# Performance work log

Hardware: AMD Instinct MI355X
Metric: run time of the kernel (lower is better)

Reference implementation:

```python
import jax, jax.numpy as jnp
import numpy as np

B, T, D, H = 2, 2048, 1024, 16
STD = 0.02

def setup_inputs() -> dict:
    key = jax.random.key(0)
    ks = jax.random.split(key, 5)
    x = jax.random.normal(ks[0], (B, T, D), dtype=jnp.float32)
    Wq = jax.random.normal(ks[1], (D, D), dtype=jnp.float32) * STD
    Wk = jax.random.normal(ks[2], (D, D), dtype=jnp.float32) * STD
    Wv = jax.random.normal(ks[3], (D, D), dtype=jnp.float32) * STD
    Wo = jax.random.normal(ks[4], (D, D), dtype=jnp.float32) * STD
    z = jnp.zeros((D,), dtype=jnp.float32)
    return {"x": x, "Wq": Wq, "bq": z, "Wk": Wk, "bk": z, "Wv": Wv, "bv": z, "Wo": Wo, "bo": z}

def _split(t, h):
    b, s, dm = t.shape
    return t.reshape(b, s, h, dm // h).transpose(0, 2, 1, 3)  # (B,h,T,d)

def reference(x, Wq, bq, Wk, bk, Wv, bv, Wo, bo):
    h = H
    # linear projections (nn.Linear: y = x @ W^T + b)
    q = _split(x @ Wq.T + bq, h)
    k = _split(x @ Wk.T + bk, h)
    v = _split(x @ Wv.T + bv, h)
    d_k = k.shape[-1]
    # scaled dot-product similarities (B,h,T,T)
    sim = jnp.einsum("bhqd,bhkd->bhqk", q, k) / jnp.sqrt(jnp.float32(d_k))
    # causal mask: upper triangle (excluding diag) filled with -inf
    Tq = sim.shape[-1]
    causal = jnp.tril(jnp.ones((Tq, Tq), dtype=bool))
    sim = jnp.where(causal, sim, -jnp.inf)
    attn = jax.nn.softmax(sim, axis=-1)
    ctx = jnp.einsum("bhqk,bhkd->bhqd", attn, v)  # (B,h,T,d)
    ctx = ctx.transpose(0, 2, 1, 3).reshape(x.shape[0], x.shape[1], -1)  # (B,T,D)
    return ctx @ Wo.T + bo
```

## Files before the change

### kernel.cpp

```cpp
#include <hip/hip_runtime.h>
#include <hip/hip_bf16.h>


typedef __attribute__((ext_vector_type(8))) short bf16x8;
typedef __attribute__((ext_vector_type(4))) float f32x4;

#define QSCALE 0.18033688011f

__device__ __forceinline__ int sniff_f32(const void* p) {
    const unsigned short* u = (const unsigned short*)p;
    int c = 0;
    for (int i = 0; i < 256; ++i) {
        int e = (u[i] >> 7) & 0xFF;
        c += (e >= 0x90) ? 1 : 0;
    }
    return c > 8;
}

__device__ __forceinline__ void async_copy16(const void* g, void* l) {
    __builtin_amdgcn_global_load_lds(
        (const __attribute__((address_space(1))) void*)g,
        (__attribute__((address_space(3))) void*)l, 16, 0, 0);
}

struct Cvt { const void* src; __hip_bfloat16* dst; int n; };
struct CvtPack { Cvt a[9]; };

__global__ __launch_bounds__(256) void cvt_bf16(CvtPack pk) {
    const Cvt c = pk.a[blockIdx.y];
    const int f32 = sniff_f32(c.src);
    const int stride = gridDim.x * 256 * 8;
    for (int idx = (blockIdx.x * 256 + threadIdx.x) * 8; idx < c.n; idx += stride) {
        if (f32) {
            const float* s = (const float*)c.src + idx;
            f32x4 a0 = *(const f32x4*)s;
            f32x4 a1 = *(const f32x4*)(s + 4);
            union { __hip_bfloat16 h[8]; bf16x8 v; } u;
#pragma unroll
            for (int e = 0; e < 4; e++) u.h[e]     = (__hip_bfloat16)a0[e];
#pragma unroll
            for (int e = 0; e < 4; e++) u.h[4 + e] = (__hip_bfloat16)a1[e];
            *(bf16x8*)&c.dst[idx] = u.v;
        } else {
            *(bf16x8*)&c.dst[idx] = *(const bf16x8*)((const __hip_bfloat16*)c.src + idx);
        }
    }
}

template <bool OF32>
__device__ __forceinline__ void gemm_async_body(
    const __hip_bfloat16* __restrict__ A, const __hip_bfloat16* __restrict__ W,
    const __hip_bfloat16* __restrict__ bias, void* __restrict__ C,
    int M, int N, int K, int bm, int bn, float outscale,
    __hip_bfloat16* sA, __hip_bfloat16* sB)
{
    const int tid  = threadIdx.x;
    const int wave = tid >> 6;
    const int lane = tid & 63;
    const int quad = lane >> 4;
    const int l15  = lane & 15;
    const int wr   = wave >> 1;
    const int wc   = wave & 1;

    const int srow = wave * 16 + (lane >> 2);
    const int scol = (lane & 3) * 8;
    const __hip_bfloat16* gA0 = A + (size_t)(bm + srow) * K + scol;
    const __hip_bfloat16* gB0 = W + (size_t)(bn + srow) * K + scol;
    __hip_bfloat16* sA0 = sA + wave * 512;
    __hip_bfloat16* sB0 = sB + wave * 512;

    f32x4 acc[4][4];
#pragma unroll
    for (int i = 0; i < 4; i++)
#pragma unroll
        for (int j = 0; j < 4; j++) acc[i][j] = (f32x4)0.0f;

    for (int k0 = 0; k0 < K; k0 += 32) {
        __syncthreads();
#pragma unroll
        for (int r = 0; r < 2; r++) {
            async_copy16(gA0 + (size_t)r * 64 * K + k0, sA0 + r * 2048);
            async_copy16(gB0 + (size_t)r * 64 * K + k0, sB0 + r * 2048);
        }
        __syncthreads();

        bf16x8 af[4], bf[4];
#pragma unroll
        for (int i = 0; i < 4; i++)
            af[i] = *(const bf16x8*)&sA[(wr * 64 + i * 16 + l15) * 32 + quad * 8];
#pragma unroll
        for (int j = 0; j < 4; j++)
            bf[j] = *(const bf16x8*)&sB[(wc * 64 + j * 16 + l15) * 32 + quad * 8];
#pragma unroll
        for (int i = 0; i < 4; i++)
#pragma unroll
            for (int j = 0; j < 4; j++)
                acc[i][j] = __builtin_amdgcn_mfma_f32_16x16x32_bf16(af[i], bf[j], acc[i][j], 0, 0, 0);
    }

    float bv[4];
#pragma unroll
    for (int j = 0; j < 4; j++)
        bv[j] = (float)bias[bn + wc * 64 + j * 16 + l15];
#pragma unroll
    for (int i = 0; i < 4; i++) {
#pragma unroll
        for (int j = 0; j < 4; j++) {
            int col = bn + wc * 64 + j * 16 + l15;
#pragma unroll
            for (int r = 0; r < 4; r++) {
                int row = bm + wr * 64 + i * 16 + quad * 4 + r;
                float v = (acc[i][j][r] + bv[j]) * outscale;
                if (OF32) ((float*)C)[(size_t)row * N + col] = v;
                else      ((__hip_bfloat16*)C)[(size_t)row * N + col] = (__hip_bfloat16)v;
            }
        }
    }
}

__global__ __launch_bounds__(256, 2) void qkv_gemm(
    const __hip_bfloat16* __restrict__ x,
    const __hip_bfloat16* __restrict__ Wq, const __hip_bfloat16* __restrict__ bq, __hip_bfloat16* __restrict__ Q,
    const __hip_bfloat16* __restrict__ Wk, const __hip_bfloat16* __restrict__ bk, __hip_bfloat16* __restrict__ Kb,
    const __hip_bfloat16* __restrict__ Wv, const __hip_bfloat16* __restrict__ bv, __hip_bfloat16* __restrict__ V,
    int M, int N, int K)
{
    __shared__ __hip_bfloat16 sA[128 * 32];
    __shared__ __hip_bfloat16 sB[128 * 32];
    const __hip_bfloat16* Wp; const __hip_bfloat16* bp; __hip_bfloat16* Cp; float sc;
    if (blockIdx.z == 0)      { Wp = Wq; bp = bq; Cp = Q;  sc = QSCALE; }
    else if (blockIdx.z == 1) { Wp = Wk; bp = bk; Cp = Kb; sc = 1.0f; }
    else                      { Wp = Wv; bp = bv; Cp = V;  sc = 1.0f; }
    gemm_async_body<false>(x, Wp, bp, Cp, M, N, K,
                           blockIdx.x * 128, blockIdx.y * 128, sc, sA, sB);
}

__global__ __launch_bounds__(256, 2) void out_gemm(
    const __hip_bfloat16* __restrict__ A, const __hip_bfloat16* __restrict__ W,
    const __hip_bfloat16* __restrict__ bias, const void* __restrict__ origW,
    void* __restrict__ C, int M, int N, int K)
{
    __shared__ __hip_bfloat16 sA[128 * 32];
    __shared__ __hip_bfloat16 sB[128 * 32];
    __shared__ int f32flag;
    if (threadIdx.x == 0) f32flag = sniff_f32(origW);
    __syncthreads();
    if (f32flag)
        gemm_async_body<true>(A, W, bias, C, M, N, K,
                              blockIdx.x * 128, blockIdx.y * 128, 1.0f, sA, sB);
    else
        gemm_async_body<false>(A, W, bias, C, M, N, K,
                               blockIdx.x * 128, blockIdx.y * 128, 1.0f, sA, sB);
}

__global__ __launch_bounds__(256, 2) void transpose_v(
    const __hip_bfloat16* __restrict__ V, __hip_bfloat16* __restrict__ VT,
    int T, int D, int H)
{
    __shared__ __hip_bfloat16 sT[64 * 72];
    const int tid = threadIdx.x;
    const int t0  = blockIdx.x * 64;
    const int h   = blockIdx.y;
    const int b   = blockIdx.z;

    for (int i = tid; i < 512; i += 256) {
        int t = i >> 3, d8 = (i & 7) * 8;
        *(bf16x8*)&sT[t * 72 + d8] =
            *(const bf16x8*)&V[((size_t)b * T + t0 + t) * D + h * 64 + d8];
    }
    __syncthreads();
    for (int i = tid; i < 512; i += 256) {
        int d = i >> 3, t8 = (i & 7) * 8;
        union { __hip_bfloat16 h[8]; bf16x8 v; } u;
#pragma unroll
        for (int e = 0; e < 8; e++) u.h[e] = sT[(t8 + e) * 72 + d];
        *(bf16x8*)&VT[(((size_t)b * H + h) * 64 + d) * T + t0 + t8] = u.v;
    }
}

#define PAD 68

__device__ __forceinline__ void tile_step(
    const __hip_bfloat16* __restrict__ sQx, __hip_bfloat16* __restrict__ sPw,
    const bf16x8 kfrag[2][4], const bf16x8 vfrag[2][4],
    f32x4 acc[4], float lacc[4],
    int diag, int wave, int quad, int l15)
{
    f32x4 s[4];
#pragma unroll
    for (int j = 0; j < 4; j++) s[j] = (f32x4)0.0f;
#pragma unroll
    for (int kk = 0; kk < 2; kk++) {
        bf16x8 a = *(const bf16x8*)&sQx[(wave * 16 + l15) * PAD + kk * 32 + quad * 8];
#pragma unroll
        for (int j = 0; j < 4; j++)
            s[j] = __builtin_amdgcn_mfma_f32_16x16x32_bf16(a, kfrag[kk][j], s[j], 0, 0, 0);
    }
    if (diag) {
        const int qrow = wave * 16 + quad * 4;
#pragma unroll
        for (int j = 0; j < 4; j++) {
            int key = j * 16 + l15;
#pragma unroll
            for (int r = 0; r < 4; r++)
                if (key > qrow + r) s[j][r] = -1e30f;
        }
    }
#pragma unroll
    for (int j = 0; j < 4; j++) {
#pragma unroll
        for (int r = 0; r < 4; r++) {
            float p = exp2f(s[j][r]);
            lacc[r] += p;
            sPw[(quad * 4 + r) * PAD + j * 16 + l15] = (__hip_bfloat16)p;
        }
    }
#pragma unroll
    for (int kk = 0; kk < 2; kk++) {
        bf16x8 a = *(const bf16x8*)&sPw[l15 * PAD + kk * 32 + quad * 8];
#pragma unroll
        for (int j = 0; j < 4; j++)
            acc[j] = __builtin_amdgcn_mfma_f32_16x16x32_bf16(a, vfrag[kk][j], acc[j], 0, 0, 0);
    }
}

__global__ __launch_bounds__(256, 2) void attn_causal(
    const __hip_bfloat16* __restrict__ Q,
    const __hip_bfloat16* __restrict__ K,
    const __hip_bfloat16* __restrict__ VT,
    __hip_bfloat16* __restrict__ O,
    int T, int D, int H)
{
    __shared__ __hip_bfloat16 sQ[2][64 * PAD];
    __shared__ __hip_bfloat16 sK[64 * PAD];
    __shared__ __hip_bfloat16 sVT[64 * PAD];
    __shared__ __hip_bfloat16 sP[4][16 * PAD];

    const int tid  = threadIdx.x;
    const int wave = tid >> 6;
    const int lane = tid & 63;
    const int quad = lane >> 4;
    const int l15  = lane & 15;

    const int NT  = T >> 6;
    const int p   = blockIdx.x;
    const int qtA = p;
    const int qtB = NT - 1 - p;
    const int h   = blockIdx.y;
    const int b   = blockIdx.z;
    const size_t headoff = (size_t)b * T * D + (size_t)h * 64;
    const size_t vtoff   = ((size_t)b * H + h) * 64 * (size_t)T;

    for (int i = tid; i < 1024; i += 256) {
        int tile = i >> 9, ii = i & 511;
        int row = ii >> 3, c8 = ii & 7;
        int qt = tile ? qtB : qtA;
        *(bf16x8*)&sQ[tile][row * PAD + c8 * 8] =
            *(const bf16x8*)&Q[headoff + (size_t)(qt * 64 + row) * D + c8 * 8];
    }

    f32x4 accA[4], accB[4];
#pragma unroll
    for (int j = 0; j < 4; j++) { accA[j] = (f32x4)0.0f; accB[j] = (f32x4)0.0f; }
    float lA[4] = {0.f, 0.f, 0.f, 0.f}, lB[4] = {0.f, 0.f, 0.f, 0.f};

    const int srow = tid >> 3;
    const int sc8  = (tid & 7) * 8;

    bf16x8 pk[2], pv[2];
#pragma unroll
    for (int u = 0; u < 2; u++) {
        int row = srow + u * 32;
        pk[u] = *(const bf16x8*)&K[headoff + (size_t)row * D + sc8];
        pv[u] = *(const bf16x8*)&VT[vtoff + (size_t)row * T + sc8];
    }

    for (int kt = 0; kt <= qtB; ++kt) {
        __syncthreads();
#pragma unroll
        for (int u = 0; u < 2; u++) {
            int row = srow + u * 32;
            *(bf16x8*)&sK[row * PAD + sc8]  = pk[u];
            *(bf16x8*)&sVT[row * PAD + sc8] = pv[u];
        }
        if (kt < qtB) {
#pragma unroll
            for (int u = 0; u < 2; u++) {
                int row = srow + u * 32;
                pk[u] = *(const bf16x8*)&K[headoff + (size_t)((kt + 1) * 64 + row) * D + sc8];
                pv[u] = *(const bf16x8*)&VT[vtoff + (size_t)row * T + (kt + 1) * 64 + sc8];
            }
        }
        __syncthreads();

        bf16x8 kfrag[2][4], vfrag[2][4];
#pragma unroll
        for (int kk = 0; kk < 2; kk++)
#pragma unroll
            for (int j = 0; j < 4; j++) {
                kfrag[kk][j] = *(const bf16x8*)&sK[(j * 16 + l15) * PAD + kk * 32 + quad * 8];
                vfrag[kk][j] = *(const bf16x8*)&sVT[(j * 16 + l15) * PAD + kk * 32 + quad * 8];
            }

        tile_step(sQ[1], sP[wave], kfrag, vfrag, accB, lB, kt == qtB, wave, quad, l15);
        if (kt <= qtA)
            tile_step(sQ[0], sP[wave], kfrag, vfrag, accA, lA, kt == qtA, wave, quad, l15);
    }

#pragma unroll
    for (int o = 1; o < 16; o <<= 1)
#pragma unroll
        for (int r = 0; r < 4; r++) {
            lA[r] += __shfl_xor(lA[r], o, 64);
            lB[r] += __shfl_xor(lB[r], o, 64);
        }

#pragma unroll
    for (int r = 0; r < 4; r++) {
        float iA = 1.0f / lA[r], iB = 1.0f / lB[r];
        int rowA = qtA * 64 + wave * 16 + quad * 4 + r;
        int rowB = qtB * 64 + wave * 16 + quad * 4 + r;
#pragma unroll
        for (int j = 0; j < 4; j++) {
            int col = j * 16 + l15;
            O[headoff + (size_t)rowA * D + col] = (__hip_bfloat16)(accA[j][r] * iA);
            O[headoff + (size_t)rowB * D + col] = (__hip_bfloat16)(accB[j][r] * iB);
        }
    }
}

extern "C" void kernel_launch(void* const* d_in, const int* in_sizes, int n_in,
                              void* d_out, int out_size, void* d_ws, size_t ws_size,
                              hipStream_t stream) {
    const int Bb = 2, T = 2048, D = 1024, H = 16;
    const int M = Bb * T;

    __hip_bfloat16* w = (__hip_bfloat16*)d_ws;
    __hip_bfloat16* Q   = w;
    __hip_bfloat16* Kb  = Q   + (size_t)M * D;
    __hip_bfloat16* Vb  = Kb  + (size_t)M * D;
    __hip_bfloat16* ctx = Vb  + (size_t)M * D;
    __hip_bfloat16* VT  = ctx + (size_t)M * D;
    __hip_bfloat16* xb  = VT  + (size_t)M * D;
    __hip_bfloat16* Wqb = xb  + (size_t)M * D;
    __hip_bfloat16* Wkb = Wqb + (size_t)D * D;
    __hip_bfloat16* Wvb = Wkb + (size_t)D * D;
    __hip_bfloat16* Wob = Wvb + (size_t)D * D;
    __hip_bfloat16* bqb = Wob + (size_t)D * D;
    __hip_bfloat16* bkb = bqb + D;
    __hip_bfloat16* bvb = bkb + D;
    __hip_bfloat16* bob = bvb + D;

    CvtPack pk;
    pk.a[0] = { d_in[0], xb,  M * D };
    pk.a[1] = { d_in[1], Wqb, D * D };
    pk.a[2] = { d_in[2], bqb, D };
    pk.a[3] = { d_in[3], Wkb, D * D };
    pk.a[4] = { d_in[4], bkb, D };
    pk.a[5] = { d_in[5], Wvb, D * D };
    pk.a[6] = { d_in[6], bvb, D };
    pk.a[7] = { d_in[7], Wob, D * D };
    pk.a[8] = { d_in[8], bob, D };

    cvt_bf16<<<dim3(512, 9), 256, 0, stream>>>(pk);
    qkv_gemm<<<dim3(M / 128, D / 128, 3), 256, 0, stream>>>(
        xb, Wqb, bqb, Q, Wkb, bkb, Kb, Wvb, bvb, Vb, M, D, D);
    transpose_v<<<dim3(T / 64, H, Bb), 256, 0, stream>>>(Vb, VT, T, D, H);
    attn_causal<<<dim3(T / 128, H, Bb), 256, 0, stream>>>(Q, Kb, VT, ctx, T, D, H);
    out_gemm<<<dim3(M / 128, D / 128), 256, 0, stream>>>(
        ctx, Wob, bob, d_in[7], d_out, M, D, D);
}
```

Baseline: 246.4 us.

## Split attention to one query tile per block and use 64-row output GEMM tiles

The causal attention kernel now handles a single 64-row query tile per block instead of a balanced pair (p, NT-1-p). That doubles the grid and raises the launch-bounds occupancy target to 4. Heads are split in two halves that walk the query tiles in opposite orders, so heavy and light blocks mix. K/V fragments are now read per MFMA rather than held in registers. The output GEMM gets a new 64x128-tile body, which doubles its block count for better CU fill, at the cost of more redundant K/V and weight loads and an uneven per-block workload in attention.

```diff
diff --git a/kernel.cpp b/kernel.cpp
--- a/kernel.cpp
+++ b/kernel.cpp
@@ -135,22 +135,88 @@
                            blockIdx.x * 128, blockIdx.y * 128, sc, sA, sB);
 }
 
+template <bool OF32>
+__device__ __forceinline__ void gemm64_body(
+    const __hip_bfloat16* __restrict__ A, const __hip_bfloat16* __restrict__ W,
+    const __hip_bfloat16* __restrict__ bias, void* __restrict__ C,
+    int M, int N, int K, int bm, int bn,
+    __hip_bfloat16* sA, __hip_bfloat16* sB)
+{
+    const int tid  = threadIdx.x;
+    const int wave = tid >> 6;
+    const int lane = tid & 63;
+    const int quad = lane >> 4;
+    const int l15  = lane & 15;
+
+    const int srow = wave * 16 + (lane >> 2);
+    const int scol = (lane & 3) * 8;
+    const __hip_bfloat16* gA0 = A + (size_t)(bm + srow) * K + scol;
+    const __hip_bfloat16* gB0 = W + (size_t)(bn + srow) * K + scol;
+    __hip_bfloat16* sA0 = sA + wave * 512;
+    __hip_bfloat16* sB0 = sB + wave * 512;
+
+    f32x4 acc[4][2];
+#pragma unroll
+    for (int i = 0; i < 4; i++)
+#pragma unroll
+        for (int j = 0; j < 2; j++) acc[i][j] = (f32x4)0.0f;
+
+    for (int k0 = 0; k0 < K; k0 += 32) {
+        __syncthreads();
+        async_copy16(gA0 + k0, sA0);
+#pragma unroll
+        for (int r = 0; r < 2; r++)
+            async_copy16(gB0 + (size_t)r * 64 * K + k0, sB0 + r * 2048);
+        __syncthreads();
+
+        bf16x8 af[4], bf[2];
+#pragma unroll
+        for (int i = 0; i < 4; i++)
+            af[i] = *(const bf16x8*)&sA[(i * 16 + l15) * 32 + quad * 8];
+#pragma unroll
+        for (int j = 0; j < 2; j++)
+            bf[j] = *(const bf16x8*)&sB[(wave * 32 + j * 16 + l15) * 32 + quad * 8];
+#pragma unroll
+        for (int i = 0; i < 4; i++)
+#pragma unroll
+            for (int j = 0; j < 2; j++)
+                acc[i][j] = __builtin_amdgcn_mfma_f32_16x16x32_bf16(af[i], bf[j], acc[i][j], 0, 0, 0);
+    }
+
+    float bv[2];
+#pragma unroll
+    for (int j = 0; j < 2; j++)
+        bv[j] = (float)bias[bn + wave * 32 + j * 16 + l15];
+#pragma unroll
+    for (int i = 0; i < 4; i++) {
+#pragma unroll
+        for (int j = 0; j < 2; j++) {
+            int col = bn + wave * 32 + j * 16 + l15;
+#pragma unroll
+            for (int r = 0; r < 4; r++) {
+                int row = bm + i * 16 + quad * 4 + r;
+                float v = acc[i][j][r] + bv[j];
+                if (OF32) ((float*)C)[(size_t)row * N + col] = v;
+                else      ((__hip_bfloat16*)C)[(size_t)row * N + col] = (__hip_bfloat16)v;
+            }
+        }
+    }
+}
+
 __global__ __launch_bounds__(256, 2) void out_gemm(
     const __hip_bfloat16* __restrict__ A, const __hip_bfloat16* __restrict__ W,
     const __hip_bfloat16* __restrict__ bias, const void* __restrict__ origW,
     void* __restrict__ C, int M, int N, int K)
 {
-    __shared__ __hip_bfloat16 sA[128 * 32];
+    __shared__ __hip_bfloat16 sA[64 * 32];
     __shared__ __hip_bfloat16 sB[128 * 32];
     __shared__ int f32flag;
     if (threadIdx.x == 0) f32flag = sniff_f32(origW);
     __syncthreads();
     if (f32flag)
-        gemm_async_body<true>(A, W, bias, C, M, N, K,
-                              blockIdx.x * 128, blockIdx.y * 128, 1.0f, sA, sB);
+        gemm64_body<true>(A, W, bias, C, M, N, K, blockIdx.x * 64, blockIdx.y * 128, sA, sB);
     else
-        gemm_async_body<false>(A, W, bias, C, M, N, K,
-                               blockIdx.x * 128, blockIdx.y * 128, 1.0f, sA, sB);
+        gemm64_body<false>(A, W, bias, C, M, N, K, blockIdx.x * 64, blockIdx.y * 128, sA, sB);
 }
 
 __global__ __launch_bounds__(256, 2) void transpose_v(
@@ -180,58 +246,14 @@
 
 #define PAD 68
 
-__device__ __forceinline__ void tile_step(
-    const __hip_bfloat16* __restrict__ sQx, __hip_bfloat16* __restrict__ sPw,
-    const bf16x8 kfrag[2][4], const bf16x8 vfrag[2][4],
-    f32x4 acc[4], float lacc[4],
-    int diag, int wave, int quad, int l15)
-{
-    f32x4 s[4];
-#pragma unroll
-    for (int j = 0; j < 4; j++) s[j] = (f32x4)0.0f;
-#pragma unroll
-    for (int kk = 0; kk < 2; kk++) {
-        bf16x8 a = *(const bf16x8*)&sQx[(wave * 16 + l15) * PAD + kk * 32 + quad * 8];
-#pragma unroll
-        for (int j = 0; j < 4; j++)
-            s[j] = __builtin_amdgcn_mfma_f32_16x16x32_bf16(a, kfrag[kk][j], s[j], 0, 0, 0);
-    }
-    if (diag) {
-        const int qrow = wave * 16 + quad * 4;
-#pragma unroll
-        for (int j = 0; j < 4; j++) {
-            int key = j * 16 + l15;
-#pragma unroll
-            for (int r = 0; r < 4; r++)
-                if (key > qrow + r) s[j][r] = -1e30f;
-        }
-    }
-#pragma unroll
-    for (int j = 0; j < 4; j++) {
-#pragma unroll
-        for (int r = 0; r < 4; r++) {
-            float p = exp2f(s[j][r]);
-            lacc[r] += p;
-            sPw[(quad * 4 + r) * PAD + j * 16 + l15] = (__hip_bfloat16)p;
-        }
-    }
-#pragma unroll
-    for (int kk = 0; kk < 2; kk++) {
-        bf16x8 a = *(const bf16x8*)&sPw[l15 * PAD + kk * 32 + quad * 8];
-#pragma unroll
-        for (int j = 0; j < 4; j++)
-            acc[j] = __builtin_amdgcn_mfma_f32_16x16x32_bf16(a, vfrag[kk][j], acc[j], 0, 0, 0);
-    }
-}
-
-__global__ __launch_bounds__(256, 2) void attn_causal(
+__global__ __launch_bounds__(256, 4) void attn_causal(
     const __hip_bfloat16* __restrict__ Q,
     const __hip_bfloat16* __restrict__ K,
     const __hip_bfloat16* __restrict__ VT,
     __hip_bfloat16* __restrict__ O,
     int T, int D, int H)
 {
-    __shared__ __hip_bfloat16 sQ[2][64 * PAD];
+    __shared__ __hip_bfloat16 sQ[64 * PAD];
     __shared__ __hip_bfloat16 sK[64 * PAD];
     __shared__ __hip_bfloat16 sVT[64 * PAD];
     __shared__ __hip_bfloat16 sP[4][16 * PAD];
@@ -242,27 +264,23 @@
     const int quad = lane >> 4;
     const int l15  = lane & 15;
 
-    const int NT  = T >> 6;
-    const int p   = blockIdx.x;
-    const int qtA = p;
-    const int qtB = NT - 1 - p;
-    const int h   = blockIdx.y;
-    const int b   = blockIdx.z;
+    const int NT = T >> 6;
+    const int qt = ((blockIdx.y >> 3) & 1) ? (NT - 1 - (int)blockIdx.x) : (int)blockIdx.x;
+    const int h  = blockIdx.y;
+    const int b  = blockIdx.z;
     const size_t headoff = (size_t)b * T * D + (size_t)h * 64;
     const size_t vtoff   = ((size_t)b * H + h) * 64 * (size_t)T;
 
-    for (int i = tid; i < 1024; i += 256) {
-        int tile = i >> 9, ii = i & 511;
-        int row = ii >> 3, c8 = ii & 7;
-        int qt = tile ? qtB : qtA;
-        *(bf16x8*)&sQ[tile][row * PAD + c8 * 8] =
+    for (int i = tid; i < 512; i += 256) {
+        int row = i >> 3, c8 = i & 7;
+        *(bf16x8*)&sQ[row * PAD + c8 * 8] =
             *(const bf16x8*)&Q[headoff + (size_t)(qt * 64 + row) * D + c8 * 8];
     }
 
-    f32x4 accA[4], accB[4];
-#pragma unroll
-    for (int j = 0; j < 4; j++) { accA[j] = (f32x4)0.0f; accB[j] = (f32x4)0.0f; }
-    float lA[4] = {0.f, 0.f, 0.f, 0.f}, lB[4] = {0.f, 0.f, 0.f, 0.f};
+    f32x4 acc_o[4];
+#pragma unroll
+    for (int j = 0; j < 4; j++) acc_o[j] = (f32x4)0.0f;
+    float lacc[4] = {0.f, 0.f, 0.f, 0.f};
 
     const int srow = tid >> 3;
     const int sc8  = (tid & 7) * 8;
@@ -275,7 +293,7 @@
         pv[u] = *(const bf16x8*)&VT[vtoff + (size_t)row * T + sc8];
     }
 
-    for (int kt = 0; kt <= qtB; ++kt) {
+    for (int kt = 0; kt <= qt; ++kt) {
         __syncthreads();
 #pragma unroll
         for (int u = 0; u < 2; u++) {
@@ -283,7 +301,7 @@
             *(bf16x8*)&sK[row * PAD + sc8]  = pk[u];
             *(bf16x8*)&sVT[row * PAD + sc8] = pv[u];
         }
-        if (kt < qtB) {
+        if (kt < qt) {
 #pragma unroll
             for (int u = 0; u < 2; u++) {
                 int row = srow + u * 32;
@@ -293,38 +311,64 @@
         }
         __syncthreads();
 
-        bf16x8 kfrag[2][4], vfrag[2][4];
-#pragma unroll
-        for (int kk = 0; kk < 2; kk++)
+        f32x4 s[4];
+#pragma unroll
+        for (int j = 0; j < 4; j++) s[j] = (f32x4)0.0f;
+#pragma unroll
+        for (int kk = 0; kk < 2; kk++) {
+            bf16x8 a = *(const bf16x8*)&sQ[(wave * 16 + l15) * PAD + kk * 32 + quad * 8];
 #pragma unroll
             for (int j = 0; j < 4; j++) {
-                kfrag[kk][j] = *(const bf16x8*)&sK[(j * 16 + l15) * PAD + kk * 32 + quad * 8];
-                vfrag[kk][j] = *(const bf16x8*)&sVT[(j * 16 + l15) * PAD + kk * 32 + quad * 8];
-            }
-
-        tile_step(sQ[1], sP[wave], kfrag, vfrag, accB, lB, kt == qtB, wave, quad, l15);
-        if (kt <= qtA)
-            tile_step(sQ[0], sP[wave], kfrag, vfrag, accA, lA, kt == qtA, wave, quad, l15);
+                bf16x8 bk8 = *(const bf16x8*)&sK[(j * 16 + l15) * PAD + kk * 32 + quad * 8];
+                s[j] = __builtin_amdgcn_mfma_f32_16x16x32_bf16(a, bk8, s[j], 0, 0, 0);
+            }
+        }
+
+        if (kt == qt) {
+            const int qrow = wave * 16 + quad * 4;
+#pragma unroll
+            for (int j = 0; j < 4; j++) {
+                int key = j * 16 + l15;
+#pragma unroll
+                for (int r = 0; r < 4; r++)
+                    if (key > qrow + r) s[j][r] = -1e30f;
+            }
+        }
+
+#pragma unroll
+        for (int j = 0; j < 4; j++) {
+#pragma unroll
+            for (int r = 0; r < 4; r++) {
+                float p = exp2f(s[j][r]);
+                lacc[r] += p;
+                sP[wave][(quad * 4 + r) * PAD + j * 16 + l15] = (__hip_bfloat16)p;
+            }
+        }
+#pragma unroll
+        for (int kk = 0; kk < 2; kk++) {
+            bf16x8 a = *(const bf16x8*)&sP[wave][l15 * PAD + kk * 32 + quad * 8];
+#pragma unroll
+            for (int j = 0; j < 4; j++) {
+                bf16x8 bv8 = *(const bf16x8*)&sVT[(j * 16 + l15) * PAD + kk * 32 + quad * 8];
+                acc_o[j] = __builtin_amdgcn_mfma_f32_16x16x32_bf16(a, bv8, acc_o[j], 0, 0, 0);
+            }
+        }
     }
 
 #pragma unroll
     for (int o = 1; o < 16; o <<= 1)
 #pragma unroll
-        for (int r = 0; r < 4; r++) {
-            lA[r] += __shfl_xor(lA[r], o, 64);
-            lB[r] += __shfl_xor(lB[r], o, 64);
-        }
+        for (int r = 0; r < 4; r++)
+            lacc[r] += __shfl_xor(lacc[r], o, 64);
 
 #pragma unroll
     for (int r = 0; r < 4; r++) {
-        float iA = 1.0f / lA[r], iB = 1.0f / lB[r];
-        int rowA = qtA * 64 + wave * 16 + quad * 4 + r;
-        int rowB = qtB * 64 + wave * 16 + quad * 4 + r;
+        float inv = 1.0f / lacc[r];
+        int row = qt * 64 + wave * 16 + quad * 4 + r;
 #pragma unroll
         for (int j = 0; j < 4; j++) {
             int col = j * 16 + l15;
-            O[headoff + (size_t)rowA * D + col] = (__hip_bfloat16)(accA[j][r] * iA);
-            O[headoff + (size_t)rowB * D + col] = (__hip_bfloat16)(accB[j][r] * iB);
+            O[headoff + (size_t)row * D + col] = (__hip_bfloat16)(acc_o[j][r] * inv);
         }
     }
 }
@@ -366,7 +410,7 @@
     qkv_gemm<<<dim3(M / 128, D / 128, 3), 256, 0, stream>>>(
         xb, Wqb, bqb, Q, Wkb, bkb, Kb, Wvb, bvb, Vb, M, D, D);
     transpose_v<<<dim3(T / 64, H, Bb), 256, 0, stream>>>(Vb, VT, T, D, H);
-    attn_causal<<<dim3(T / 128, H, Bb), 256, 0, stream>>>(Q, Kb, VT, ctx, T, D, H);
-    out_gemm<<<dim3(M / 128, D / 128), 256, 0, stream>>>(
+    attn_causal<<<dim3(T / 64, H, Bb), 256, 0, stream>>>(Q, Kb, VT, ctx, T, D, H);
+    out_gemm<<<dim3(M / 64, D / 128), 256, 0, stream>>>(
         ctx, Wob, bob, d_in[7], d_out, M, D, D);
 }
```

Result: faster. 221.8 us (-10.0%).
